# Kernel tuning notes

Hardware: AMD Instinct MI355X
Metric: run time of the kernel (lower is better)

The kernel has to match this reference:

```python
import jax, jax.numpy as jnp
import numpy as np
from jax import lax

DIM = 64


def _dwconv(x, w, b):
    # x: [B,C,H,W], w: [C,1,kh,kw] depthwise, 'same' padding
    kh, kw = w.shape[2], w.shape[3]
    y = lax.conv_general_dilated(
        x, w, window_strides=(1, 1),
        padding=[(kh // 2, kh // 2), (kw // 2, kw // 2)],
        dimension_numbers=("NCHW", "OIHW", "NCHW"),
        feature_group_count=x.shape[1])
    return y + b[None, :, None, None]


def _conv1x1(x, w, b):
    y = lax.conv_general_dilated(
        x, w, window_strides=(1, 1), padding="VALID",
        dimension_numbers=("NCHW", "OIHW", "NCHW"))
    return y + b[None, :, None, None]


def _avgpool3(x):
    # PyTorch AvgPool2d(3,1,1) default count_include_pad=True -> sum/9
    s = lax.reduce_window(x, 0.0, lax.add, (1, 1, 3, 3), (1, 1, 1, 1),
                          [(0, 0), (0, 0), (1, 1), (1, 1)])
    return s / 9.0


def _maxpool3(x):
    return lax.reduce_window(x, -jnp.inf, lax.max, (1, 1, 3, 3), (1, 1, 1, 1),
                             [(0, 0), (0, 0), (1, 1), (1, 1)])


def setup_inputs() -> dict:
    key = jax.random.key(0)
    ks = jax.random.split(key, 18)
    C = DIM
    def w(k, shape):
        fan_in = shape[1] * shape[2] * shape[3]
        bound = 1.0 / np.sqrt(fan_in)
        return jax.random.uniform(k, shape, jnp.float32, -bound, bound)
    def b(k, fan_in):
        bound = 1.0 / np.sqrt(fan_in)
        return jax.random.uniform(k, (C,), jnp.float32, -bound, bound)
    return {
        "x": jax.random.normal(ks[0], (16, C, 128, 128), jnp.float32),
        "w55": w(ks[1], (C, 1, 5, 5)), "b55": b(ks[2], 25),
        "w17_0": w(ks[3], (C, 1, 1, 7)), "b17_0": b(ks[4], 7),
        "w17_1": w(ks[5], (C, 1, 7, 1)), "b17_1": b(ks[6], 7),
        "w111_0": w(ks[7], (C, 1, 1, 11)), "b111_0": b(ks[8], 11),
        "w111_1": w(ks[9], (C, 1, 11, 1)), "b111_1": b(ks[10], 11),
        "w211_0": w(ks[11], (C, 1, 1, 21)), "b211_0": b(ks[12], 21),
        "w211_1": w(ks[13], (C, 1, 21, 1)), "b211_1": b(ks[14], 21),
        "w11": w(ks[15], (C, C, 1, 1)), "b11": b(ks[16], C),
    }


def reference(x, w55, b55, w17_0, b17_0, w17_1, b17_1,
              w111_0, b111_0, w111_1, b111_1,
              w211_0, b211_0, w211_1, b211_1, w11, b11):
    def branch(inp):
        c55 = _dwconv(inp, w55, b55)
        c17 = _dwconv(_dwconv(inp, w17_0, b17_0), w17_1, b17_1)
        c111 = _dwconv(_dwconv(inp, w111_0, b111_0), w111_1, b111_1)
        c211 = _dwconv(_dwconv(inp, w211_0, b211_0), w211_1, b211_1)
        return _conv1x1(c55 + c17 + c111 + c211, w11, b11)

    mixer = branch(x)
    mixer_1 = branch(_avgpool3(x))
    mixer_2 = branch(_maxpool3(x))
    return (mixer + mixer_1 + mixer_2) * x
```

## Files before the change

### kernel.cpp

```cpp
#include <hip/hip_runtime.h>
#include <hip/hip_bf16.h>
#include <cstdint>

#define HH 128
#define WW 128
#define CC 64
#define BB 16
#define PLANE (HH*WW)
#define TPSTR 16512

#define XS_STR    52
#define XRAW_STR  60
#define XSTH_H    8736
#define H7_H      11328
#define UNION_F   7072
#define H11_H     14144
#define H21_H     16960
#define SMEM_FLOATS 12232

__device__ __forceinline__ float lo16(unsigned int u) {
  return __uint_as_float(u << 16);
}
__device__ __forceinline__ float hi16(unsigned int u) {
  return __uint_as_float(u & 0xffff0000u);
}

__global__ __launch_bounds__(256, 3) void k_dwsum(
    const float* __restrict__ x, float* __restrict__ T,
    const float* __restrict__ w55, const float* __restrict__ b55,
    const float* __restrict__ w17_0, const float* __restrict__ b17_0,
    const float* __restrict__ w17_1, const float* __restrict__ b17_1,
    const float* __restrict__ w111_0, const float* __restrict__ b111_0,
    const float* __restrict__ w111_1, const float* __restrict__ b111_1,
    const float* __restrict__ w211_0, const float* __restrict__ b211_0,
    const float* __restrict__ w211_1, const float* __restrict__ b211_1) {
  __shared__ float sm[SMEM_FLOATS];
  __hip_bfloat16* hb = (__hip_bfloat16*)sm;

  const int bid = blockIdx.x;
  const int pl = bid >> 3;
  const int t = bid & 7;
  const int tR0 = (t >> 2) * 64;
  const int tC0 = (t & 3) * 32;
  const int ch = pl & (CC - 1);
  const float* xp = x + (size_t)pl * PLANE;
  float* Tp = T + (size_t)pl * TPSTR;
  const int tid = threadIdx.x;

  {
    float* xraw = sm + UNION_F;
    const int base_r = tR0 - 11, base_c = tC0 - 12;
    for (int i = tid; i < 86 * 14; i += 256) {
      int rr = i / 14;
      int jj = i - rr * 14;
      int gr = base_r + rr;
      int gc = base_c + jj * 4;
      float4 v = make_float4(0.f, 0.f, 0.f, 0.f);
      if ((unsigned)gr < 128u && (unsigned)gc < 128u)
        v = *(const float4*)(xp + gr * WW + gc);
      *(float4*)(xraw + rr * XRAW_STR + jj * 4) = v;
    }
  }
  __syncthreads();

  {
    const float* xraw = sm + UNION_F;
    __hip_bfloat16* xsTh = hb + XSTH_H;
    for (int i = tid; i < 28 * 13; i += 256) {
      int rg = i % 28;
      int jj = i / 28;
      int rr0 = rg * 3;
      const float* rp = xraw + rr0 * XRAW_STR + jj * 4;
      float w[5][8];
      #pragma unroll
      for (int k = 0; k < 5; ++k) {
        float4 a = *(const float4*)(rp + k * XRAW_STR);
        float4 b = *(const float4*)(rp + k * XRAW_STR + 4);
        w[k][0] = a.x; w[k][1] = a.y; w[k][2] = a.z; w[k][3] = a.w;
        w[k][4] = b.x; w[k][5] = b.y; w[k][6] = b.z; w[k][7] = b.w;
      }
      int gc0 = tC0 + jj * 4 - 12;
      bool cv[7];
      #pragma unroll
      for (int p = 1; p <= 6; ++p) cv[p] = (unsigned)(gc0 + p) < 128u;

      #pragma unroll
      for (int k = 0; k < 3; ++k) {
        int rr = rr0 + k;
        int gr = tR0 + rr - 10;
        bool rv0 = (unsigned)(gr - 1) < 128u;
        bool rv1 = (unsigned)(gr) < 128u;
        bool rv2 = (unsigned)(gr + 1) < 128u;
        float M0[7], M1[7], M2[7];
        #pragma unroll
        for (int p = 1; p <= 6; ++p) {
          M0[p] = (rv0 && cv[p]) ? w[k][p] : -3.402823466e38f;
          M1[p] = (rv1 && cv[p]) ? w[k + 1][p] : -3.402823466e38f;
          M2[p] = (rv2 && cv[p]) ? w[k + 2][p] : -3.402823466e38f;
        }
        float uq[4];
        #pragma unroll
        for (int q = 0; q < 4; ++q) {
          float s = w[k][q + 1] + w[k][q + 2] + w[k][q + 3] + w[k + 1][q + 1] +
                    w[k + 1][q + 2] + w[k + 1][q + 3] + w[k + 2][q + 1] +
                    w[k + 2][q + 2] + w[k + 2][q + 3];
          float m = fmaxf(
              fmaxf(fmaxf(M0[q + 1], M0[q + 2]), fmaxf(M0[q + 3], M1[q + 1])),
              fmaxf(fmaxf(M1[q + 2], M1[q + 3]),
                    fmaxf(fmaxf(M2[q + 1], M2[q + 2]), M2[q + 3])));
          float val = w[k + 1][q + 2] + s * (1.f / 9.f) + m;
          bool vo = rv1 && ((unsigned)(gc0 + q + 2) < 128u);
          uq[q] = vo ? val : 0.f;
        }
        *(float4*)(sm + rr * XS_STR + jj * 4) =
            make_float4(uq[0], uq[1], uq[2], uq[3]);
        int rt = rr - 8;
        if ((unsigned)rt < 68u) {
          #pragma unroll
          for (int q = 0; q < 4; ++q) {
            int ct = jj * 4 + q - 8;
            if ((unsigned)ct < 36u)
              xsTh[ct * 72 + rt] = __float2bfloat16(uq[q]);
          }
        }
      }
    }
  }

  float k7[7], k11[11], k21[21];
  #pragma unroll
  for (int i = 0; i < 7; ++i) k7[i] = w17_0[ch * 7 + i];
  #pragma unroll
  for (int i = 0; i < 11; ++i) k11[i] = w111_0[ch * 11 + i];
  #pragma unroll
  for (int i = 0; i < 21; ++i) k21[i] = w211_0[ch * 21 + i];
  float bb7 = 3.f * b17_0[ch];
  float bb11 = 3.f * b111_0[ch];
  float bb21 = 3.f * b211_0[ch];

  __syncthreads();

  for (int it = tid; it < 84 * 4; it += 256) {
    int rr = it % 84;
    int cg = it / 84;
    float w[28];
    const float* xr = sm + rr * XS_STR + cg * 8;
    #pragma unroll
    for (int j = 0; j < 7; ++j) {
      float4 v = *(const float4*)(xr + 4 * j);
      w[4 * j] = v.x; w[4 * j + 1] = v.y; w[4 * j + 2] = v.z; w[4 * j + 3] = v.w;
    }
    int gr = tR0 + rr - 10;
    bool rv = (unsigned)gr < 128u;
    bool v11r = (rr >= 5) && (rr <= 78);
    bool v7r = (rr >= 7) && (rr <= 76);
    #pragma unroll
    for (int j = 0; j < 8; ++j) {
      float a21 = bb21, a11 = bb11, a7 = bb7;
      #pragma unroll
      for (int d = 0; d < 21; ++d) a21 += k21[d] * w[j + d];
      #pragma unroll
      for (int d = 0; d < 11; ++d) a11 += k11[d] * w[j + 5 + d];
      #pragma unroll
      for (int d = 0; d < 7; ++d) a7 += k7[d] * w[j + 7 + d];
      int c = cg * 8 + j;
      hb[H21_H + c * 88 + rr] = __float2bfloat16(rv ? a21 : 0.f);
      if (v11r) hb[H11_H + c * 88 + rr - 5] = __float2bfloat16(rv ? a11 : 0.f);
      if (v7r) hb[H7_H + c * 88 + rr - 7] = __float2bfloat16(rv ? a7 : 0.f);
    }
  }

  float v7a[7], v11a[11], v21a[21], w5a[25];
  #pragma unroll
  for (int i = 0; i < 7; ++i) v7a[i] = w17_1[ch * 7 + i];
  #pragma unroll
  for (int i = 0; i < 11; ++i) v11a[i] = w111_1[ch * 11 + i];
  #pragma unroll
  for (int i = 0; i < 21; ++i) v21a[i] = w211_1[ch * 21 + i];
  #pragma unroll
  for (int i = 0; i < 25; ++i) w5a[i] = w55[ch * 25 + i];
  float bsum = 3.f * (b55[ch] + b17_1[ch] + b111_1[ch] + b211_1[ch]);

  __syncthreads();

  {
    int c = tid & 31;
    int r0 = (tid >> 5) * 8;
    float acc[8];
    #pragma unroll
    for (int j = 0; j < 8; ++j) acc[j] = bsum;

    float A[28];
    {
      const unsigned* p = (const unsigned*)&hb[H21_H + c * 88 + r0];
      uint4 q0 = *(const uint4*)p;
      uint4 q1 = *(const uint4*)(p + 4);
      uint4 q2 = *(const uint4*)(p + 8);
      uint2 q3 = *(const uint2*)(p + 12);
      A[0]=lo16(q0.x);A[1]=hi16(q0.x);A[2]=lo16(q0.y);A[3]=hi16(q0.y);
      A[4]=lo16(q0.z);A[5]=hi16(q0.z);A[6]=lo16(q0.w);A[7]=hi16(q0.w);
      A[8]=lo16(q1.x);A[9]=hi16(q1.x);A[10]=lo16(q1.y);A[11]=hi16(q1.y);
      A[12]=lo16(q1.z);A[13]=hi16(q1.z);A[14]=lo16(q1.w);A[15]=hi16(q1.w);
      A[16]=lo16(q2.x);A[17]=hi16(q2.x);A[18]=lo16(q2.y);A[19]=hi16(q2.y);
      A[20]=lo16(q2.z);A[21]=hi16(q2.z);A[22]=lo16(q2.w);A[23]=hi16(q2.w);
      A[24]=lo16(q3.x);A[25]=hi16(q3.x);A[26]=lo16(q3.y);A[27]=hi16(q3.y);
      #pragma unroll
      for (int d = 0; d < 21; ++d)
        #pragma unroll
        for (int j = 0; j < 8; ++j) acc[j] += v21a[d] * A[d + j];
    }
    {
      const unsigned* p = (const unsigned*)&hb[H11_H + c * 88 + r0];
      uint4 q0 = *(const uint4*)p;
      uint4 q1 = *(const uint4*)(p + 4);
      uint2 q2 = *(const uint2*)(p + 8);
      A[0]=lo16(q0.x);A[1]=hi16(q0.x);A[2]=lo16(q0.y);A[3]=hi16(q0.y);
      A[4]=lo16(q0.z);A[5]=hi16(q0.z);A[6]=lo16(q0.w);A[7]=hi16(q0.w);
      A[8]=lo16(q1.x);A[9]=hi16(q1.x);A[10]=lo16(q1.y);A[11]=hi16(q1.y);
      A[12]=lo16(q1.z);A[13]=hi16(q1.z);A[14]=lo16(q1.w);A[15]=hi16(q1.w);
      A[16]=lo16(q2.x);A[17]=hi16(q2.x);
      #pragma unroll
      for (int d = 0; d < 11; ++d)
        #pragma unroll
        for (int j = 0; j < 8; ++j) acc[j] += v11a[d] * A[d + j];
    }
    {
      const unsigned* p = (const unsigned*)&hb[H7_H + c * 88 + r0];
      uint4 q0 = *(const uint4*)p;
      uint4 q1 = *(const uint4*)(p + 4);
      A[0]=lo16(q0.x);A[1]=hi16(q0.x);A[2]=lo16(q0.y);A[3]=hi16(q0.y);
      A[4]=lo16(q0.z);A[5]=hi16(q0.z);A[6]=lo16(q0.w);A[7]=hi16(q0.w);
      A[8]=lo16(q1.x);A[9]=hi16(q1.x);A[10]=lo16(q1.y);A[11]=hi16(q1.y);
      A[12]=lo16(q1.z);A[13]=hi16(q1.z);
      #pragma unroll
      for (int d = 0; d < 7; ++d)
        #pragma unroll
        for (int j = 0; j < 8; ++j) acc[j] += v7a[d] * A[d + j];
    }
    {
      #pragma unroll
      for (int dc = 0; dc < 5; ++dc) {
        const unsigned* p = (const unsigned*)&hb[XSTH_H + (c + dc) * 72 + r0];
        uint4 q0 = *(const uint4*)p;
        uint2 q1 = *(const uint2*)(p + 4);
        float X[12];
        X[0]=lo16(q0.x);X[1]=hi16(q0.x);X[2]=lo16(q0.y);X[3]=hi16(q0.y);
        X[4]=lo16(q0.z);X[5]=hi16(q0.z);X[6]=lo16(q0.w);X[7]=hi16(q0.w);
        X[8]=lo16(q1.x);X[9]=hi16(q1.x);X[10]=lo16(q1.y);X[11]=hi16(q1.y);
        #pragma unroll
        for (int dr = 0; dr < 5; ++dr)
          #pragma unroll
          for (int j = 0; j < 8; ++j) acc[j] += w5a[dr * 5 + dc] * X[j + dr];
      }
    }
    #pragma unroll
    for (int j = 0; j < 8; ++j)
      Tp[(size_t)(tR0 + r0 + j) * WW + tC0 + c] = acc[j];
  }
}

__global__ __launch_bounds__(256) void k_mix(const float* __restrict__ T,
                                             const float* __restrict__ x,
                                             const float* __restrict__ w11,
                                             const float* __restrict__ b11,
                                             float* __restrict__ out) {
  __shared__ float Wt[64 * 68];
  int bid = blockIdx.x;
  int b = bid >> 7;
  int px0 = (bid & 127) * 128;
  int tid = threadIdx.x;

  for (int i = tid; i < 4096; i += 256) {
    int co = i >> 6, ci = i & 63;
    Wt[ci * 68 + co] = w11[i];
  }
  __syncthreads();

  int pxg = tid & 31;
  int cog = tid >> 5;
  const float* Tb = T + (size_t)b * 64 * TPSTR + px0 + pxg * 4;
  const float* wp = Wt + cog * 8;

  float acc[8][4];
  #pragma unroll
  for (int a = 0; a < 8; ++a)
    #pragma unroll
    for (int p = 0; p < 4; ++p) acc[a][p] = 0.f;

  float4 tb[3][4];
  #pragma unroll
  for (int kk = 0; kk < 4; ++kk)
    tb[0][kk] = *(const float4*)(Tb + (size_t)kk * TPSTR);
  #pragma unroll
  for (int kk = 0; kk < 4; ++kk)
    tb[1][kk] = *(const float4*)(Tb + (size_t)(4 + kk) * TPSTR);

  #pragma unroll
  for (int kc = 0; kc < 16; ++kc) {
    const int cur = kc % 3;
    if (kc < 14) {
      const int nxt = (kc + 2) % 3;
      #pragma unroll
      for (int kk = 0; kk < 4; ++kk)
        tb[nxt][kk] =
            *(const float4*)(Tb + (size_t)((kc + 2) * 4 + kk) * TPSTR);
    }
    #pragma unroll
    for (int kk = 0; kk < 4; ++kk) {
      int k = kc * 4 + kk;
      float4 q0 = *(const float4*)(wp + k * 68);
      float4 q1 = *(const float4*)(wp + k * 68 + 4);
      float wf[8] = {q0.x, q0.y, q0.z, q0.w, q1.x, q1.y, q1.z, q1.w};
      float4 tv = tb[cur][kk];
      float tvv[4] = {tv.x, tv.y, tv.z, tv.w};
      #pragma unroll
      for (int a = 0; a < 8; ++a)
        #pragma unroll
        for (int p = 0; p < 4; ++p) acc[a][p] += wf[a] * tvv[p];
    }
  }

  const float* xb = x + (size_t)b * (CC * PLANE) + px0 + pxg * 4;
  float* ob = out + (size_t)b * (CC * PLANE) + px0 + pxg * 4;
  #pragma unroll
  for (int a = 0; a < 8; ++a) {
    int co = cog * 8 + a;
    float bb = 3.f * b11[co];
    float4 xv = *(const float4*)(xb + (size_t)co * PLANE);
    float4 o;
    o.x = (acc[a][0] + bb) * xv.x;
    o.y = (acc[a][1] + bb) * xv.y;
    o.z = (acc[a][2] + bb) * xv.z;
    o.w = (acc[a][3] + bb) * xv.w;
    *(float4*)(ob + (size_t)co * PLANE) = o;
  }
}

extern "C" void kernel_launch(void* const* d_in, const int* in_sizes, int n_in,
                              void* d_out, int out_size, void* d_ws,
                              size_t ws_size, hipStream_t stream) {
  const float* x = (const float*)d_in[0];
  const float* w55 = (const float*)d_in[1];
  const float* b55 = (const float*)d_in[2];
  const float* w17_0 = (const float*)d_in[3];
  const float* b17_0 = (const float*)d_in[4];
  const float* w17_1 = (const float*)d_in[5];
  const float* b17_1 = (const float*)d_in[6];
  const float* w111_0 = (const float*)d_in[7];
  const float* b111_0 = (const float*)d_in[8];
  const float* w111_1 = (const float*)d_in[9];
  const float* b111_1 = (const float*)d_in[10];
  const float* w211_0 = (const float*)d_in[11];
  const float* b211_0 = (const float*)d_in[12];
  const float* w211_1 = (const float*)d_in[13];
  const float* b211_1 = (const float*)d_in[14];
  const float* w11 = (const float*)d_in[15];
  const float* b11 = (const float*)d_in[16];
  float* outp = (float*)d_out;

  float* T = (float*)d_ws;

  k_dwsum<<<BB * CC * 8, 256, 0, stream>>>(
      x, T, w55, b55, w17_0, b17_0, w17_1, b17_1, w111_0, b111_0, w111_1,
      b111_1, w211_0, b211_0, w211_1, b211_1);
  k_mix<<<BB * 128, 256, 0, stream>>>(T, x, w11, b11, outp);
}
```

Baseline: 300.5 us.

## Split pooled-input stage into two passes, fast interior path, retile mix kernel

Measured after the change: 717.5 us. +138.8%, slower.

```diff
diff --git a/kernel.cpp b/kernel.cpp
--- a/kernel.cpp
+++ b/kernel.cpp
@@ -16,7 +16,7 @@
 #define UNION_F   7072
 #define H11_H     14144
 #define H21_H     16960
-#define SMEM_FLOATS 12232
+#define SMEM_FLOATS 9888
 
 __device__ __forceinline__ float lo16(unsigned int u) {
   return __uint_as_float(u << 16);
@@ -25,7 +25,121 @@
   return __uint_as_float(u & 0xffff0000u);
 }
 
-__global__ __launch_bounds__(256, 3) void k_dwsum(
+__device__ __forceinline__ void a2_store(float* sm, __hip_bfloat16* xsTh,
+                                         int rr, int jj, const float uq[4]) {
+  *(float4*)(sm + rr * XS_STR + jj * 4) =
+      make_float4(uq[0], uq[1], uq[2], uq[3]);
+  int rt = rr - 8;
+  if ((unsigned)rt < 68u) {
+    #pragma unroll
+    for (int q = 0; q < 4; ++q) {
+      int ct = jj * 4 + q - 8;
+      if ((unsigned)ct < 36u)
+        xsTh[ct * 72 + rt] = __float2bfloat16(uq[q]);
+    }
+  }
+}
+
+__device__ __forceinline__ void a2_item_fast(float* sm, __hip_bfloat16* xsTh,
+                                             const float* xbuf, int rg,
+                                             int jj, int roff) {
+  int rr0 = rg * 3;
+  const float* rp = xbuf + (rr0 - roff) * XRAW_STR + jj * 4;
+  float w[5][8];
+  #pragma unroll
+  for (int k = 0; k < 5; ++k) {
+    float4 a = *(const float4*)(rp + k * XRAW_STR);
+    float4 b = *(const float4*)(rp + k * XRAW_STR + 4);
+    w[k][0] = a.x; w[k][1] = a.y; w[k][2] = a.z; w[k][3] = a.w;
+    w[k][4] = b.x; w[k][5] = b.y; w[k][6] = b.z; w[k][7] = b.w;
+  }
+  float cs[3][7], cm[3][7];
+  #pragma unroll
+  for (int p = 1; p <= 6; ++p) {
+    float a0 = w[0][p], a1 = w[1][p], a2 = w[2][p], a3 = w[3][p],
+          a4 = w[4][p];
+    float s12 = a1 + a2;
+    cs[0][p] = a0 + s12;
+    cs[1][p] = s12 + a3;
+    float s34 = a3 + a4;
+    cs[2][p] = a2 + s34;
+    float m12 = fmaxf(a1, a2);
+    cm[0][p] = fmaxf(a0, m12);
+    cm[1][p] = fmaxf(m12, a3);
+    float m34 = fmaxf(a3, a4);
+    cm[2][p] = fmaxf(a2, m34);
+  }
+  #pragma unroll
+  for (int k = 0; k < 3; ++k) {
+    float t23 = cs[k][2] + cs[k][3];
+    float t45 = cs[k][4] + cs[k][5];
+    float n23 = fmaxf(cm[k][2], cm[k][3]);
+    float n45 = fmaxf(cm[k][4], cm[k][5]);
+    float uq[4];
+    uq[0] = w[k + 1][2] + (cs[k][1] + t23) * (1.f / 9.f) +
+            fmaxf(cm[k][1], n23);
+    uq[1] = w[k + 1][3] + (t23 + cs[k][4]) * (1.f / 9.f) +
+            fmaxf(n23, cm[k][4]);
+    uq[2] = w[k + 1][4] + (cs[k][3] + t45) * (1.f / 9.f) +
+            fmaxf(cm[k][3], n45);
+    uq[3] = w[k + 1][5] + (t45 + cs[k][6]) * (1.f / 9.f) +
+            fmaxf(n45, cm[k][6]);
+    a2_store(sm, xsTh, rr0 + k, jj, uq);
+  }
+}
+
+__device__ __forceinline__ void a2_item_slow(float* sm, __hip_bfloat16* xsTh,
+                                             const float* xbuf, int tR0,
+                                             int tC0, int rg, int jj,
+                                             int roff) {
+  int rr0 = rg * 3;
+  const float* rp = xbuf + (rr0 - roff) * XRAW_STR + jj * 4;
+  float w[5][8];
+  #pragma unroll
+  for (int k = 0; k < 5; ++k) {
+    float4 a = *(const float4*)(rp + k * XRAW_STR);
+    float4 b = *(const float4*)(rp + k * XRAW_STR + 4);
+    w[k][0] = a.x; w[k][1] = a.y; w[k][2] = a.z; w[k][3] = a.w;
+    w[k][4] = b.x; w[k][5] = b.y; w[k][6] = b.z; w[k][7] = b.w;
+  }
+  int gc0 = tC0 + jj * 4 - 12;
+  bool cv[7];
+  #pragma unroll
+  for (int p = 1; p <= 6; ++p) cv[p] = (unsigned)(gc0 + p) < 128u;
+
+  #pragma unroll
+  for (int k = 0; k < 3; ++k) {
+    int rr = rr0 + k;
+    int gr = tR0 + rr - 10;
+    bool rv0 = (unsigned)(gr - 1) < 128u;
+    bool rv1 = (unsigned)(gr) < 128u;
+    bool rv2 = (unsigned)(gr + 1) < 128u;
+    float M0[7], M1[7], M2[7];
+    #pragma unroll
+    for (int p = 1; p <= 6; ++p) {
+      M0[p] = (rv0 && cv[p]) ? w[k][p] : -3.402823466e38f;
+      M1[p] = (rv1 && cv[p]) ? w[k + 1][p] : -3.402823466e38f;
+      M2[p] = (rv2 && cv[p]) ? w[k + 2][p] : -3.402823466e38f;
+    }
+    float uq[4];
+    #pragma unroll
+    for (int q = 0; q < 4; ++q) {
+      float s = w[k][q + 1] + w[k][q + 2] + w[k][q + 3] + w[k + 1][q + 1] +
+                w[k + 1][q + 2] + w[k + 1][q + 3] + w[k + 2][q + 1] +
+                w[k + 2][q + 2] + w[k + 2][q + 3];
+      float m = fmaxf(
+          fmaxf(fmaxf(M0[q + 1], M0[q + 2]), fmaxf(M0[q + 3], M1[q + 1])),
+          fmaxf(fmaxf(M1[q + 2], M1[q + 3]),
+                fmaxf(fmaxf(M2[q + 1], M2[q + 2]), M2[q + 3])));
+      float val = w[k + 1][q + 2] + s * (1.f / 9.f) + m;
+      bool vo = rv1 && ((unsigned)(gc0 + q + 2) < 128u);
+      uq[q] = vo ? val : 0.f;
+    }
+    a2_store(sm, xsTh, rr, jj, uq);
+  }
+}
+
+__global__ __launch_bounds__(256, 4) void k_dwsum(
     const float* __restrict__ x, float* __restrict__ T,
     const float* __restrict__ w55, const float* __restrict__ b55,
     const float* __restrict__ w17_0, const float* __restrict__ b17_0,
@@ -47,84 +161,54 @@
   float* Tp = T + (size_t)pl * TPSTR;
   const int tid = threadIdx.x;
 
-  {
-    float* xraw = sm + UNION_F;
-    const int base_r = tR0 - 11, base_c = tC0 - 12;
-    for (int i = tid; i < 86 * 14; i += 256) {
+  float* xbuf = sm + UNION_F;
+  __hip_bfloat16* xsTh = hb + XSTH_H;
+  const int base_r = tR0 - 11, base_c = tC0 - 12;
+
+  int nbrJ = 0, brJ0 = 0;
+  if (tC0 == 0) { nbrJ = 3; brJ0 = 0; }
+  if (tC0 == 96) { nbrJ = 3; brJ0 = 10; }
+
+  #pragma unroll
+  for (int pass = 0; pass < 2; ++pass) {
+    const int roff = pass * 42;
+    const int rg_lo = pass * 14;
+    for (int i = tid; i < 44 * 14; i += 256) {
       int rr = i / 14;
       int jj = i - rr * 14;
-      int gr = base_r + rr;
+      int gr = base_r + roff + rr;
       int gc = base_c + jj * 4;
       float4 v = make_float4(0.f, 0.f, 0.f, 0.f);
       if ((unsigned)gr < 128u && (unsigned)gc < 128u)
         v = *(const float4*)(xp + gr * WW + gc);
-      *(float4*)(xraw + rr * XRAW_STR + jj * 4) = v;
-    }
-  }
-  __syncthreads();
-
-  {
-    const float* xraw = sm + UNION_F;
-    __hip_bfloat16* xsTh = hb + XSTH_H;
-    for (int i = tid; i < 28 * 13; i += 256) {
-      int rg = i % 28;
-      int jj = i / 28;
-      int rr0 = rg * 3;
-      const float* rp = xraw + rr0 * XRAW_STR + jj * 4;
-      float w[5][8];
-      #pragma unroll
-      for (int k = 0; k < 5; ++k) {
-        float4 a = *(const float4*)(rp + k * XRAW_STR);
-        float4 b = *(const float4*)(rp + k * XRAW_STR + 4);
-        w[k][0] = a.x; w[k][1] = a.y; w[k][2] = a.z; w[k][3] = a.w;
-        w[k][4] = b.x; w[k][5] = b.y; w[k][6] = b.z; w[k][7] = b.w;
+      *(float4*)(xbuf + rr * XRAW_STR + jj * 4) = v;
+    }
+    __syncthreads();
+    for (int i = tid; i < 14 * 13; i += 256) {
+      int rg = rg_lo + (i % 14);
+      int jj = i / 14;
+      a2_item_fast(sm, xsTh, xbuf, rg, jj, roff);
+    }
+    __syncthreads();
+    int nbrR = 0, brR0 = 0;
+    if (pass == 0 && tR0 == 0) { nbrR = 4; brR0 = 0; }
+    if (pass == 1 && tR0 == 64) { nbrR = 4; brR0 = 10; }
+    int nA = nbrR * 13;
+    int nfix = nA + (14 - nbrR) * nbrJ;
+    for (int i = tid; i < nfix; i += 256) {
+      int rgl, jj;
+      if (i < nA) {
+        rgl = brR0 + i / 13;
+        jj = i % 13;
+      } else {
+        int i2 = i - nA;
+        jj = brJ0 + i2 % 3;
+        int r = i2 / 3;
+        rgl = (nbrR != 0 && brR0 == 0) ? (r + 4) : r;
       }
-      int gc0 = tC0 + jj * 4 - 12;
-      bool cv[7];
-      #pragma unroll
-      for (int p = 1; p <= 6; ++p) cv[p] = (unsigned)(gc0 + p) < 128u;
-
-      #pragma unroll
-      for (int k = 0; k < 3; ++k) {
-        int rr = rr0 + k;
-        int gr = tR0 + rr - 10;
-        bool rv0 = (unsigned)(gr - 1) < 128u;
-        bool rv1 = (unsigned)(gr) < 128u;
-        bool rv2 = (unsigned)(gr + 1) < 128u;
-        float M0[7], M1[7], M2[7];
-        #pragma unroll
-        for (int p = 1; p <= 6; ++p) {
-          M0[p] = (rv0 && cv[p]) ? w[k][p] : -3.402823466e38f;
-          M1[p] = (rv1 && cv[p]) ? w[k + 1][p] : -3.402823466e38f;
-          M2[p] = (rv2 && cv[p]) ? w[k + 2][p] : -3.402823466e38f;
-        }
-        float uq[4];
-        #pragma unroll
-        for (int q = 0; q < 4; ++q) {
-          float s = w[k][q + 1] + w[k][q + 2] + w[k][q + 3] + w[k + 1][q + 1] +
-                    w[k + 1][q + 2] + w[k + 1][q + 3] + w[k + 2][q + 1] +
-                    w[k + 2][q + 2] + w[k + 2][q + 3];
-          float m = fmaxf(
-              fmaxf(fmaxf(M0[q + 1], M0[q + 2]), fmaxf(M0[q + 3], M1[q + 1])),
-              fmaxf(fmaxf(M1[q + 2], M1[q + 3]),
-                    fmaxf(fmaxf(M2[q + 1], M2[q + 2]), M2[q + 3])));
-          float val = w[k + 1][q + 2] + s * (1.f / 9.f) + m;
-          bool vo = rv1 && ((unsigned)(gc0 + q + 2) < 128u);
-          uq[q] = vo ? val : 0.f;
-        }
-        *(float4*)(sm + rr * XS_STR + jj * 4) =
-            make_float4(uq[0], uq[1], uq[2], uq[3]);
-        int rt = rr - 8;
-        if ((unsigned)rt < 68u) {
-          #pragma unroll
-          for (int q = 0; q < 4; ++q) {
-            int ct = jj * 4 + q - 8;
-            if ((unsigned)ct < 36u)
-              xsTh[ct * 72 + rt] = __float2bfloat16(uq[q]);
-          }
-        }
-      }
-    }
+      a2_item_slow(sm, xsTh, xbuf, tR0, tC0, rg_lo + rgl, jj, roff);
+    }
+    __syncthreads();
   }
 
   float k7[7], k11[11], k21[21];
@@ -138,35 +222,52 @@
   float bb11 = 3.f * b111_0[ch];
   float bb21 = 3.f * b211_0[ch];
 
-  __syncthreads();
-
-  for (int it = tid; it < 84 * 4; it += 256) {
-    int rr = it % 84;
-    int cg = it / 84;
-    float w[28];
-    const float* xr = sm + rr * XS_STR + cg * 8;
-    #pragma unroll
-    for (int j = 0; j < 7; ++j) {
-      float4 v = *(const float4*)(xr + 4 * j);
-      w[4 * j] = v.x; w[4 * j + 1] = v.y; w[4 * j + 2] = v.z; w[4 * j + 3] = v.w;
-    }
-    int gr = tR0 + rr - 10;
-    bool rv = (unsigned)gr < 128u;
-    bool v11r = (rr >= 5) && (rr <= 78);
-    bool v7r = (rr >= 7) && (rr <= 76);
-    #pragma unroll
-    for (int j = 0; j < 8; ++j) {
-      float a21 = bb21, a11 = bb11, a7 = bb7;
-      #pragma unroll
-      for (int d = 0; d < 21; ++d) a21 += k21[d] * w[j + d];
-      #pragma unroll
-      for (int d = 0; d < 11; ++d) a11 += k11[d] * w[j + 5 + d];
-      #pragma unroll
-      for (int d = 0; d < 7; ++d) a7 += k7[d] * w[j + 7 + d];
-      int c = cg * 8 + j;
-      hb[H21_H + c * 88 + rr] = __float2bfloat16(rv ? a21 : 0.f);
-      if (v11r) hb[H11_H + c * 88 + rr - 5] = __float2bfloat16(rv ? a11 : 0.f);
-      if (v7r) hb[H7_H + c * 88 + rr - 7] = __float2bfloat16(rv ? a7 : 0.f);
+  {
+    const int rlo = (tR0 == 0) ? 10 : 0;
+    const int ilo = (tR0 == 0) ? 0 : 74;
+    for (int it = tid; it < 336; it += 256) {
+      if (it < 296) {
+        int rr = rlo + it % 74;
+        int cg = it / 74;
+        float w[28];
+        const float* xr = sm + rr * XS_STR + cg * 8;
+        #pragma unroll
+        for (int j = 0; j < 7; ++j) {
+          float4 v = *(const float4*)(xr + 4 * j);
+          w[4 * j] = v.x; w[4 * j + 1] = v.y;
+          w[4 * j + 2] = v.z; w[4 * j + 3] = v.w;
+        }
+        bool v11r = (rr >= 5) && (rr <= 78);
+        bool v7r = (rr >= 7) && (rr <= 76);
+        #pragma unroll
+        for (int j = 0; j < 8; ++j) {
+          float a21 = bb21, a11 = bb11, a7 = bb7;
+          #pragma unroll
+          for (int d = 0; d < 21; ++d) a21 += k21[d] * w[j + d];
+          #pragma unroll
+          for (int d = 0; d < 11; ++d) a11 += k11[d] * w[j + 5 + d];
+          #pragma unroll
+          for (int d = 0; d < 7; ++d) a7 += k7[d] * w[j + 7 + d];
+          int c = cg * 8 + j;
+          hb[H21_H + c * 88 + rr] = __float2bfloat16(a21);
+          if (v11r) hb[H11_H + c * 88 + rr - 5] = __float2bfloat16(a11);
+          if (v7r) hb[H7_H + c * 88 + rr - 7] = __float2bfloat16(a7);
+        }
+      } else {
+        int i2 = it - 296;
+        int rr = ilo + i2 % 10;
+        int cg = i2 / 10;
+        bool v11r = (rr >= 5) && (rr <= 78);
+        bool v7r = (rr >= 7) && (rr <= 76);
+        __hip_bfloat16 z = __float2bfloat16(0.f);
+        #pragma unroll
+        for (int j = 0; j < 8; ++j) {
+          int c = cg * 8 + j;
+          hb[H21_H + c * 88 + rr] = z;
+          if (v11r) hb[H11_H + c * 88 + rr - 5] = z;
+          if (v7r) hb[H7_H + c * 88 + rr - 7] = z;
+        }
+      }
     }
   }
 
@@ -259,72 +360,74 @@
   }
 }
 
-__global__ __launch_bounds__(256) void k_mix(const float* __restrict__ T,
-                                             const float* __restrict__ x,
-                                             const float* __restrict__ w11,
-                                             const float* __restrict__ b11,
-                                             float* __restrict__ out) {
+__global__ __launch_bounds__(256, 4) void k_mix(const float* __restrict__ T,
+                                                const float* __restrict__ x,
+                                                const float* __restrict__ w11,
+                                                const float* __restrict__ b11,
+                                                float* __restrict__ out) {
   __shared__ float Wt[64 * 68];
+
   int bid = blockIdx.x;
-  int b = bid >> 7;
-  int px0 = (bid & 127) * 128;
+  int b = bid >> 6;
+  int px0 = (bid & 63) * 256;
   int tid = threadIdx.x;
 
   for (int i = tid; i < 4096; i += 256) {
     int co = i >> 6, ci = i & 63;
     Wt[ci * 68 + co] = w11[i];
   }
+
+  int pxg = tid & 63;
+  int cog = tid >> 6;
+  const float* Tb = T + (size_t)b * 64 * TPSTR + px0 + pxg * 4;
+  const float* wp = Wt + cog * 16;
+
+  float4 tb0[4], tb1[4];
+  #pragma unroll
+  for (int kk = 0; kk < 4; ++kk)
+    tb0[kk] = *(const float4*)(Tb + (size_t)kk * TPSTR);
+
   __syncthreads();
 
-  int pxg = tid & 31;
-  int cog = tid >> 5;
-  const float* Tb = T + (size_t)b * 64 * TPSTR + px0 + pxg * 4;
-  const float* wp = Wt + cog * 8;
-
-  float acc[8][4];
-  #pragma unroll
-  for (int a = 0; a < 8; ++a)
+  float acc[16][4];
+  #pragma unroll
+  for (int a = 0; a < 16; ++a)
     #pragma unroll
     for (int p = 0; p < 4; ++p) acc[a][p] = 0.f;
 
-  float4 tb[3][4];
-  #pragma unroll
-  for (int kk = 0; kk < 4; ++kk)
-    tb[0][kk] = *(const float4*)(Tb + (size_t)kk * TPSTR);
-  #pragma unroll
-  for (int kk = 0; kk < 4; ++kk)
-    tb[1][kk] = *(const float4*)(Tb + (size_t)(4 + kk) * TPSTR);
-
   #pragma unroll
   for (int kc = 0; kc < 16; ++kc) {
-    const int cur = kc % 3;
-    if (kc < 14) {
-      const int nxt = (kc + 2) % 3;
+    float4* cur = (kc & 1) ? tb1 : tb0;
+    float4* nxt = (kc & 1) ? tb0 : tb1;
+    if (kc < 15) {
       #pragma unroll
       for (int kk = 0; kk < 4; ++kk)
-        tb[nxt][kk] =
-            *(const float4*)(Tb + (size_t)((kc + 2) * 4 + kk) * TPSTR);
+        nxt[kk] = *(const float4*)(Tb + (size_t)(kc * 4 + 4 + kk) * TPSTR);
     }
     #pragma unroll
     for (int kk = 0; kk < 4; ++kk) {
       int k = kc * 4 + kk;
-      float4 q0 = *(const float4*)(wp + k * 68);
-      float4 q1 = *(const float4*)(wp + k * 68 + 4);
-      float wf[8] = {q0.x, q0.y, q0.z, q0.w, q1.x, q1.y, q1.z, q1.w};
-      float4 tv = tb[cur][kk];
+      const float* wr = wp + k * 68;
+      float4 tv = cur[kk];
       float tvv[4] = {tv.x, tv.y, tv.z, tv.w};
       #pragma unroll
-      for (int a = 0; a < 8; ++a)
-        #pragma unroll
-        for (int p = 0; p < 4; ++p) acc[a][p] += wf[a] * tvv[p];
+      for (int g = 0; g < 4; ++g) {
+        float4 qg = *(const float4*)(wr + g * 4);
+        float wf4[4] = {qg.x, qg.y, qg.z, qg.w};
+        #pragma unroll
+        for (int a = 0; a < 4; ++a)
+          #pragma unroll
+          for (int p = 0; p < 4; ++p)
+            acc[g * 4 + a][p] += wf4[a] * tvv[p];
+      }
     }
   }
 
   const float* xb = x + (size_t)b * (CC * PLANE) + px0 + pxg * 4;
   float* ob = out + (size_t)b * (CC * PLANE) + px0 + pxg * 4;
   #pragma unroll
-  for (int a = 0; a < 8; ++a) {
-    int co = cog * 8 + a;
+  for (int a = 0; a < 16; ++a) {
+    int co = cog * 16 + a;
     float bb = 3.f * b11[co];
     float4 xv = *(const float4*)(xb + (size_t)co * PLANE);
     float4 o;
@@ -363,5 +466,5 @@
   k_dwsum<<<BB * CC * 8, 256, 0, stream>>>(
       x, T, w55, b55, w17_0, b17_0, w17_1, b17_1, w111_0, b111_0, w111_1,
       b111_1, w211_0, b211_0, w211_1, b211_1);
-  k_mix<<<BB * 128, 256, 0, stream>>>(T, x, w11, b11, outp);
-}
+  k_mix<<<BB * 64, 256, 0, stream>>>(T, x, w11, b11, outp);
+}
```
